# Kernel tuning notes

Measured on AMD Instinct MI355X. Metric: run time of the kernel, lower is better.

## Reference

```python
import jax, jax.numpy as jnp
import numpy as np

D, C, N = 128, 128, 1000000
NUM_PLACES = 5000
TOPK = 10
MIN_SIM = 0.8
MIN_VOTES = 0.0


def setup_inputs() -> dict:
    key = jax.random.key(0)
    k1, k2, k3, k4, k5, k6 = jax.random.split(key, 6)
    final_boxes = jax.random.uniform(k1, (D, 4), dtype=jnp.float32)
    final_scores = jax.random.uniform(k2, (D,), dtype=jnp.float32)
    final_classes = jax.random.randint(k3, (D,), 0, 80, dtype=jnp.int64)
    descriptors = jax.random.normal(k4, (D, C), dtype=jnp.float32)
    X = jax.random.normal(k5, (N, C), dtype=jnp.float32)
    place_ids = jax.random.randint(k6, (N, 1), 0, NUM_PLACES).astype(jnp.float32)
    places_db = jnp.concatenate([X, place_ids], axis=1)  # (N, C+1)
    return {
        "final_boxes": final_boxes,
        "final_scores": final_scores,
        "final_classes": final_classes,
        "descriptors": descriptors,
        "places_db": places_db,
    }


def reference(final_boxes, final_scores, final_classes, descriptors, places_db):
    X = places_db[:, :-1]                       # (N, C)
    idx = places_db[:, -1].astype(jnp.int32)    # (N,) place ids

    sims = jnp.matmul(descriptors, X.T)         # (D, N)  -- dominant traffic
    top_sims, top_idx = jax.lax.top_k(sims, TOPK)  # (D, K)

    places = idx[top_idx]                       # (D, K) place ids of neighbors
    mask = top_sims >= MIN_SIM                  # (D, K) accepted neighbors

    # per-row vote counts: for each kept entry i, count kept entries with same id
    eq = places[:, :, None] == places[:, None, :]          # (D, K, K)
    counts = jnp.sum(eq & mask[:, None, :], axis=2)        # (D, K)
    counts = jnp.where(mask, counts, 0)

    max_count = counts.max(axis=1)                          # (D,)
    n_kept = mask.sum(axis=1)                               # (D,)

    # torch.unique sorts ids ascending, counts.argmax picks first max ->
    # tie-break by smallest place id among entries with max count
    BIG = jnp.int32(2**30)
    cand = mask & (counts == max_count[:, None])
    majority = jnp.where(cand, places, BIG).min(axis=1)     # (D,)

    vote_ratio = max_count.astype(jnp.float32) / jnp.maximum(n_kept, 1).astype(jnp.float32)
    valid = (n_kept > 0) & (vote_ratio >= MIN_VOTES)

    classes_out = jnp.where(valid, majority, -1).astype(jnp.int64)

    # similarity score: max top_sim whose neighbor id equals the majority
    # (over ALL topk entries, regardless of min_sim mask, as in original)
    match = places == jnp.where(valid, majority, -1)[:, None]
    NEG = jnp.float32(-1e30)
    best = jnp.where(match, top_sims, NEG).max(axis=1)
    scores_out = jnp.where(valid & match.any(axis=1), best, 0.0).astype(jnp.float32)

    return final_boxes, scores_out, classes_out
```

## Files before the change

kernel.cpp:

```cpp
#include <hip/hip_runtime.h>
#include <stdint.h>

#define DQ 128
#define CDIM 128
#define ROW_F 129
#define N_DB 1000000
#define CHUNK 32
#define NCHUNK (N_DB / CHUNK)
#define GRIDF 768
#define NTHRF 256
#define CHUNK_FLOATS (CHUNK * ROW_F)
#define WAVE_SLOTS 258
#define BF_STRIDE 136
#define BFB_SHORTS (CHUNK * BF_STRIDE)
#define CAP 512
#define NTOP 10
#define MIN_SIM_F 0.8f

typedef __attribute__((ext_vector_type(8))) short bf16x8;
typedef __attribute__((ext_vector_type(4))) float f32x4;
typedef __attribute__((ext_vector_type(4))) uint32_t u32x4;

#define AS1 __attribute__((address_space(1)))
#define AS3 __attribute__((address_space(3)))

__device__ __forceinline__ short f2bf_rne(float x) {
  uint32_t u = __float_as_uint(x);
  u += 0x7FFFu + ((u >> 16) & 1u);
  return (short)(u >> 16);
}

__device__ __forceinline__ void stage32(const float* __restrict__ src,
                                        float* scr, int w, int lane) {
  const int base = w * WAVE_SLOTS;
#pragma unroll
  for (int k = 0; k < 4; ++k) {
    const int s = base + 64 * k + lane;
    __builtin_amdgcn_global_load_lds((const AS1 void*)(src + 4 * s),
                                     (AS3 void*)(scr + 4 * (base + 64 * k)),
                                     16, 0, 0);
  }
  if (lane < 2) {
    const int s = base + 256 + lane;
    __builtin_amdgcn_global_load_lds((const AS1 void*)(src + 4 * s),
                                     (AS3 void*)(scr + 4 * (base + 256)),
                                     16, 0, 0);
  }
}

__device__ __forceinline__ void pack32(const float* scr, short* bfb, int w,
                                       int lane) {
  const int r = 8 * w + (lane >> 3);
  const int cb = lane & 7;
  const float* rp = scr + r * ROW_F + cb * 16;
  uint32_t d[8];
#pragma unroll
  for (int i = 0; i < 8; ++i) {
    const uint32_t ue = __float_as_uint(rp[2 * i]);
    const uint32_t uo = __float_as_uint(rp[2 * i + 1]);
    d[i] = __builtin_amdgcn_perm(uo, ue, 0x07060302u);
  }
  u32x4* wp = (u32x4*)(bfb + r * BF_STRIDE + cb * 16);
  wp[0] = (u32x4){d[0], d[1], d[2], d[3]};
  wp[1] = (u32x4){d[4], d[5], d[6], d[7]};
}

__global__ __launch_bounds__(NTHRF, 4) void filter_kernel(
    const float* __restrict__ desc, const float* __restrict__ pdb,
    int* __restrict__ cnt, int* __restrict__ cand) {
  __shared__ float tau_s[DQ];
  __shared__ __align__(16) float scr0[CHUNK_FLOATS];
  __shared__ __align__(16) float scr1[CHUNK_FLOATS];
  __shared__ __align__(16) short bfb0[BFB_SHORTS];
  __shared__ __align__(16) short bfb1[BFB_SHORTS];

  const int t = threadIdx.x;
  const int w = t >> 6;
  const int lane = t & 63;
  const int r16 = lane & 15;
  const int kg = lane >> 4;

  const int bid = blockIdx.x;
  const int C = (NCHUNK - bid + GRIDF - 1) / GRIDF;

  if (t < DQ) {
    const float4* dp = (const float4*)(desc + t * CDIM);
    float ssq = 0.f;
#pragma unroll
    for (int c = 0; c < 32; ++c) {
      const float4 v = dp[c];
      ssq = fmaf(v.x, v.x, ssq);
      ssq = fmaf(v.y, v.y, ssq);
      ssq = fmaf(v.z, v.z, ssq);
      ssq = fmaf(v.w, v.w, ssq);
    }
    tau_s[t] = 3.8f * sqrtf(ssq) - 2.0f;
  }

  bf16x8 afrag[2][4];
#pragma unroll
  for (int qt = 0; qt < 2; ++qt) {
    const int q = (2 * w + qt) * 16 + r16;
#pragma unroll
    for (int ks = 0; ks < 4; ++ks) {
      const float* ap = desc + q * CDIM + ks * 32 + kg * 8;
      bf16x8 a;
#pragma unroll
      for (int j = 0; j < 8; ++j) a[j] = f2bf_rne(ap[j]);
      afrag[qt][ks] = a;
    }
  }

  asm volatile("s_waitcnt vmcnt(0)" ::: "memory");

  stage32(pdb + (size_t)bid * CHUNK_FLOATS, scr0, w, lane);
  if (C > 1) {
    stage32(pdb + (size_t)(bid + GRIDF) * CHUNK_FLOATS, scr1, w, lane);
    asm volatile("s_waitcnt vmcnt(5)" ::: "memory");
  } else {
    asm volatile("s_waitcnt vmcnt(0)" ::: "memory");
  }
  pack32(scr0, bfb0, w, lane);
  asm volatile("s_waitcnt lgkmcnt(0)" ::: "memory");
  __builtin_amdgcn_s_barrier();
  asm volatile("" ::: "memory");

  float tau_l[2][4];
#pragma unroll
  for (int qt = 0; qt < 2; ++qt)
#pragma unroll
    for (int r = 0; r < 4; ++r)
      tau_l[qt][r] = tau_s[(2 * w + qt) * 16 + kg * 4 + r];

  for (int i = 0; i < C; ++i) {
    const int chunk = bid + i * GRIDF;
    float* scr_st = (i & 1) ? scr1 : scr0;
    const float* scr_pk = (i & 1) ? scr0 : scr1;
    const short* bf_cm = (i & 1) ? bfb1 : bfb0;
    short* bf_pk = (i & 1) ? bfb0 : bfb1;
    const bool have2 = (i + 2 < C);

    if (have2)
      stage32(pdb + (size_t)(chunk + 2 * GRIDF) * CHUNK_FLOATS, scr_st, w, lane);

    f32x4 acc[2][2];
    acc[0][0] = (f32x4){0.f, 0.f, 0.f, 0.f};
    acc[0][1] = (f32x4){0.f, 0.f, 0.f, 0.f};
    acc[1][0] = (f32x4){0.f, 0.f, 0.f, 0.f};
    acc[1][1] = (f32x4){0.f, 0.f, 0.f, 0.f};
#pragma unroll
    for (int ks = 0; ks < 4; ++ks) {
#pragma unroll
      for (int rt = 0; rt < 2; ++rt) {
        const bf16x8 b =
            *(const bf16x8*)(bf_cm + (rt * 16 + r16) * BF_STRIDE + ks * 32 + kg * 8);
        acc[0][rt] =
            __builtin_amdgcn_mfma_f32_16x16x32_bf16(afrag[0][ks], b, acc[0][rt], 0, 0, 0);
        acc[1][rt] =
            __builtin_amdgcn_mfma_f32_16x16x32_bf16(afrag[1][ks], b, acc[1][rt], 0, 0, 0);
      }
    }

#pragma unroll
    for (int qt = 0; qt < 2; ++qt)
#pragma unroll
      for (int rt = 0; rt < 2; ++rt)
#pragma unroll
        for (int reg = 0; reg < 4; ++reg) {
          const float sim = acc[qt][rt][reg];
          if (sim >= tau_l[qt][reg]) {
            const int q = (2 * w + qt) * 16 + kg * 4 + reg;
            const int row = chunk * CHUNK + rt * 16 + r16;
            const int pos = atomicAdd(&cnt[q], 1);
            if (pos < CAP) cand[q * CAP + pos] = row;
          }
        }

    if (have2)
      asm volatile("s_waitcnt vmcnt(5)" ::: "memory");
    else
      asm volatile("s_waitcnt vmcnt(0)" ::: "memory");

    if (i + 1 < C) pack32(scr_pk, bf_pk, w, lane);

    asm volatile("s_waitcnt lgkmcnt(0)" ::: "memory");
    __builtin_amdgcn_s_barrier();
    asm volatile("" ::: "memory");
  }
}

__global__ __launch_bounds__(512) void finalize_kernel(
    const float* __restrict__ boxes, const float* __restrict__ desc,
    const float* __restrict__ pdb, const int* __restrict__ cnt,
    const int* __restrict__ cand, float* __restrict__ out) {
  const int q = blockIdx.x;
  const int t = threadIdx.x;
  const int wav = t >> 6;
  const int lane = t & 63;
  __shared__ float dq[CDIM];
  __shared__ float simsL[CAP];
  __shared__ int idxL[CAP];

  if (t < CDIM) dq[t] = desc[q * CDIM + t];
  __syncthreads();

  int n = cnt[q];
  if (n > CAP) n = CAP;

  const float dql = dq[lane];
  const float dqh = dq[lane + 64];
  const int base_q = q * CAP;

  for (int ci0 = wav; ci0 < n; ci0 += 32) {
    int r[4];
#pragma unroll
    for (int u = 0; u < 4; ++u) {
      const int ci = ci0 + 8 * u;
      r[u] = cand[base_q + ((ci < n) ? ci : ci0)];
    }
    float a[4], b[4];
#pragma unroll
    for (int u = 0; u < 4; ++u) {
      const float* xp = pdb + (size_t)r[u] * ROW_F;
      a[u] = xp[lane];
      b[u] = xp[lane + 64];
    }
#pragma unroll
    for (int u = 0; u < 4; ++u) {
      const int ci = ci0 + 8 * u;
      float part = fmaf(dql, a[u], dqh * b[u]);
#pragma unroll
      for (int off = 32; off; off >>= 1) part += __shfl_xor(part, off);
      if (ci < n && lane == 0) {
        simsL[ci] = part;
        idxL[ci] = r[u];
      }
    }
  }
  __syncthreads();

  if (t < 4) out[q * 4 + t] = boxes[q * 4 + t];

  if (wav == 0) {
    float ts[NTOP];
    int ti[NTOP];
#pragma unroll
    for (int k = 0; k < NTOP; ++k) {
      float bv = -3e38f;
      int ba = -1;
      for (int ci = lane; ci < n; ci += 64)
        if (simsL[ci] > bv) { bv = simsL[ci]; ba = ci; }
#pragma unroll
      for (int off = 32; off; off >>= 1) {
        const float ov = __shfl_xor(bv, off);
        const int oa = __shfl_xor(ba, off);
        if (ov > bv) { bv = ov; ba = oa; }
      }
      ts[k] = bv;
      ti[k] = (ba >= 0) ? idxL[ba] : -1;
      if (lane == 0 && ba >= 0) simsL[ba] = -3e38f;
    }

    if (lane == 0) {
      int pl[NTOP];
      bool mk[NTOP];
      int n_kept = 0;
#pragma unroll
      for (int k = 0; k < NTOP; ++k) {
        pl[k] = (ti[k] >= 0) ? (int)pdb[(size_t)ti[k] * ROW_F + CDIM] : -2;
        mk[k] = (ti[k] >= 0) && (ts[k] >= MIN_SIM_F);
        n_kept += mk[k] ? 1 : 0;
      }
      int maxc = 0;
      int counts[NTOP];
#pragma unroll
      for (int j = 0; j < NTOP; ++j) {
        int cj = 0;
        if (mk[j]) {
#pragma unroll
          for (int k = 0; k < NTOP; ++k)
            if (mk[k] && pl[k] == pl[j]) cj++;
        }
        counts[j] = cj;
        if (cj > maxc) maxc = cj;
      }
      const int BIGC = 1 << 30;
      int majority = BIGC;
#pragma unroll
      for (int j = 0; j < NTOP; ++j)
        if (mk[j] && counts[j] == maxc && pl[j] < majority) majority = pl[j];
      const bool valid = (n_kept > 0);
      const int cls = valid ? majority : -1;
      bool any = false;
      float best = -3e38f;
#pragma unroll
      for (int k = 0; k < NTOP; ++k)
        if (pl[k] == cls) {
          any = true;
          if (ts[k] > best) best = ts[k];
        }
      const float score = (valid && any) ? best : 0.f;
      out[512 + q] = score;
      out[640 + q] = (float)cls;
    }
  }
}

extern "C" void kernel_launch(void* const* d_in, const int* in_sizes, int n_in,
                              void* d_out, int out_size, void* d_ws,
                              size_t ws_size, hipStream_t stream) {
  (void)in_sizes; (void)n_in; (void)out_size; (void)ws_size;
  const float* boxes = (const float*)d_in[0];
  const float* desc = (const float*)d_in[3];
  const float* pdb = (const float*)d_in[4];
  float* out = (float*)d_out;

  int* cnt = (int*)d_ws;
  int* cand = (int*)((char*)d_ws + 512);

  hipMemsetAsync(cnt, 0, DQ * sizeof(int), stream);
  filter_kernel<<<GRIDF, NTHRF, 0, stream>>>(desc, pdb, cnt, cand);
  finalize_kernel<<<DQ, 512, 0, stream>>>(boxes, desc, pdb, cnt, cand, out);
}
```

Baseline: 141.0 us.

## Stage database chunks through registers instead of direct global-to-LDS loads

Replaces the async global_load_lds staging with ordinary float4 loads into two sets of registers, prefetched two chunks ahead, which are then written to LDS scratch and packed to bf16. The main loop is unrolled by two to ping-pong register sets and LDS buffers explicitly. The first database loads are issued before the descriptor norm and fragment setup so they overlap that work. This adds register pressure, so launch bounds drop from 4 to 3 blocks per CU, and the extra LDS write and wait per chunk could reduce latency hiding.

```diff
diff --git a/kernel.cpp b/kernel.cpp
--- a/kernel.cpp
+++ b/kernel.cpp
@@ -10,7 +10,6 @@
 #define GRIDF 768
 #define NTHRF 256
 #define CHUNK_FLOATS (CHUNK * ROW_F)
-#define WAVE_SLOTS 258
 #define BF_STRIDE 136
 #define BFB_SHORTS (CHUNK * BF_STRIDE)
 #define CAP 512
@@ -21,31 +20,10 @@
 typedef __attribute__((ext_vector_type(4))) float f32x4;
 typedef __attribute__((ext_vector_type(4))) uint32_t u32x4;
 
-#define AS1 __attribute__((address_space(1)))
-#define AS3 __attribute__((address_space(3)))
-
 __device__ __forceinline__ short f2bf_rne(float x) {
   uint32_t u = __float_as_uint(x);
   u += 0x7FFFu + ((u >> 16) & 1u);
   return (short)(u >> 16);
-}
-
-__device__ __forceinline__ void stage32(const float* __restrict__ src,
-                                        float* scr, int w, int lane) {
-  const int base = w * WAVE_SLOTS;
-#pragma unroll
-  for (int k = 0; k < 4; ++k) {
-    const int s = base + 64 * k + lane;
-    __builtin_amdgcn_global_load_lds((const AS1 void*)(src + 4 * s),
-                                     (AS3 void*)(scr + 4 * (base + 64 * k)),
-                                     16, 0, 0);
-  }
-  if (lane < 2) {
-    const int s = base + 256 + lane;
-    __builtin_amdgcn_global_load_lds((const AS1 void*)(src + 4 * s),
-                                     (AS3 void*)(scr + 4 * (base + 256)),
-                                     16, 0, 0);
-  }
 }
 
 __device__ __forceinline__ void pack32(const float* scr, short* bfb, int w,
@@ -65,7 +43,65 @@
   wp[1] = (u32x4){d[4], d[5], d[6], d[7]};
 }
 
-__global__ __launch_bounds__(NTHRF, 4) void filter_kernel(
+#define LOADS(cc, R0, R1, R2, R3, RT)                                          \
+  do {                                                                         \
+    const float4* ps_ =                                                        \
+        (const float4*)(pdb + (size_t)(cc)*CHUNK_FLOATS) + 258 * w;            \
+    R0 = ps_[lane];                                                            \
+    R1 = ps_[64 + lane];                                                       \
+    R2 = ps_[128 + lane];                                                      \
+    R3 = ps_[192 + lane];                                                      \
+    if (lane < 2) RT = ps_[256 + lane];                                        \
+  } while (0)
+
+#define WRITES(scr_, R0, R1, R2, R3, RT)                                       \
+  do {                                                                         \
+    float4* qs_ = (float4*)(scr_) + 258 * w;                                   \
+    qs_[lane] = R0;                                                            \
+    qs_[64 + lane] = R1;                                                       \
+    qs_[128 + lane] = R2;                                                      \
+    qs_[192 + lane] = R3;                                                      \
+    if (lane < 2) qs_[256 + lane] = RT;                                        \
+  } while (0)
+
+#define LGKM0() asm volatile("s_waitcnt lgkmcnt(0)" ::: "memory")
+#define BARRIER()                                                              \
+  do {                                                                         \
+    __builtin_amdgcn_s_barrier();                                              \
+    asm volatile("" ::: "memory");                                             \
+  } while (0)
+
+#define COMPUTE_CHUNK(bf_cm, chunkidx)                                         \
+  do {                                                                         \
+    f32x4 acc[2][2];                                                           \
+    acc[0][0] = (f32x4){0.f, 0.f, 0.f, 0.f};                                   \
+    acc[0][1] = (f32x4){0.f, 0.f, 0.f, 0.f};                                   \
+    acc[1][0] = (f32x4){0.f, 0.f, 0.f, 0.f};                                   \
+    acc[1][1] = (f32x4){0.f, 0.f, 0.f, 0.f};                                   \
+    _Pragma("unroll") for (int ks = 0; ks < 4; ++ks) {                         \
+      _Pragma("unroll") for (int rt = 0; rt < 2; ++rt) {                       \
+        const bf16x8 b = *(const bf16x8*)((bf_cm) + (rt * 16 + r16) *          \
+                                              BF_STRIDE + ks * 32 + kg * 8);   \
+        acc[0][rt] = __builtin_amdgcn_mfma_f32_16x16x32_bf16(                  \
+            afrag[0][ks], b, acc[0][rt], 0, 0, 0);                             \
+        acc[1][rt] = __builtin_amdgcn_mfma_f32_16x16x32_bf16(                  \
+            afrag[1][ks], b, acc[1][rt], 0, 0, 0);                             \
+      }                                                                        \
+    }                                                                          \
+    _Pragma("unroll") for (int qt = 0; qt < 2; ++qt)                           \
+        _Pragma("unroll") for (int rt = 0; rt < 2; ++rt)                       \
+            _Pragma("unroll") for (int reg = 0; reg < 4; ++reg) {              \
+      const float sim = acc[qt][rt][reg];                                      \
+      if (sim >= tau_l[qt][reg]) {                                             \
+        const int q = (2 * w + qt) * 16 + kg * 4 + reg;                        \
+        const int row = (chunkidx)*CHUNK + rt * 16 + r16;                      \
+        const int pos = atomicAdd(&cnt[q], 1);                                 \
+        if (pos < CAP) cand[q * CAP + pos] = row;                              \
+      }                                                                        \
+    }                                                                          \
+  } while (0)
+
+__global__ __launch_bounds__(NTHRF, 3) void filter_kernel(
     const float* __restrict__ desc, const float* __restrict__ pdb,
     int* __restrict__ cnt, int* __restrict__ cand) {
   __shared__ float tau_s[DQ];
@@ -83,6 +119,12 @@
   const int bid = blockIdx.x;
   const int C = (NCHUNK - bid + GRIDF - 1) / GRIDF;
 
+  float4 rA0{}, rA1{}, rA2{}, rA3{}, rAt{};
+  float4 rB0{}, rB1{}, rB2{}, rB3{}, rBt{};
+
+  LOADS(bid, rA0, rA1, rA2, rA3, rAt);
+  if (C > 1) LOADS(bid + GRIDF, rB0, rB1, rB2, rB3, rBt);
+
   if (t < DQ) {
     const float4* dp = (const float4*)(desc + t * CDIM);
     float ssq = 0.f;
@@ -111,19 +153,11 @@
     }
   }
 
-  asm volatile("s_waitcnt vmcnt(0)" ::: "memory");
-
-  stage32(pdb + (size_t)bid * CHUNK_FLOATS, scr0, w, lane);
-  if (C > 1) {
-    stage32(pdb + (size_t)(bid + GRIDF) * CHUNK_FLOATS, scr1, w, lane);
-    asm volatile("s_waitcnt vmcnt(5)" ::: "memory");
-  } else {
-    asm volatile("s_waitcnt vmcnt(0)" ::: "memory");
-  }
+  WRITES(scr0, rA0, rA1, rA2, rA3, rAt);
+  LGKM0();
   pack32(scr0, bfb0, w, lane);
-  asm volatile("s_waitcnt lgkmcnt(0)" ::: "memory");
-  __builtin_amdgcn_s_barrier();
-  asm volatile("" ::: "memory");
+  LGKM0();
+  BARRIER();
 
   float tau_l[2][4];
 #pragma unroll
@@ -132,60 +166,27 @@
     for (int r = 0; r < 4; ++r)
       tau_l[qt][r] = tau_s[(2 * w + qt) * 16 + kg * 4 + r];
 
-  for (int i = 0; i < C; ++i) {
-    const int chunk = bid + i * GRIDF;
-    float* scr_st = (i & 1) ? scr1 : scr0;
-    const float* scr_pk = (i & 1) ? scr0 : scr1;
-    const short* bf_cm = (i & 1) ? bfb1 : bfb0;
-    short* bf_pk = (i & 1) ? bfb0 : bfb1;
-    const bool have2 = (i + 2 < C);
-
-    if (have2)
-      stage32(pdb + (size_t)(chunk + 2 * GRIDF) * CHUNK_FLOATS, scr_st, w, lane);
-
-    f32x4 acc[2][2];
-    acc[0][0] = (f32x4){0.f, 0.f, 0.f, 0.f};
-    acc[0][1] = (f32x4){0.f, 0.f, 0.f, 0.f};
-    acc[1][0] = (f32x4){0.f, 0.f, 0.f, 0.f};
-    acc[1][1] = (f32x4){0.f, 0.f, 0.f, 0.f};
-#pragma unroll
-    for (int ks = 0; ks < 4; ++ks) {
-#pragma unroll
-      for (int rt = 0; rt < 2; ++rt) {
-        const bf16x8 b =
-            *(const bf16x8*)(bf_cm + (rt * 16 + r16) * BF_STRIDE + ks * 32 + kg * 8);
-        acc[0][rt] =
-            __builtin_amdgcn_mfma_f32_16x16x32_bf16(afrag[0][ks], b, acc[0][rt], 0, 0, 0);
-        acc[1][rt] =
-            __builtin_amdgcn_mfma_f32_16x16x32_bf16(afrag[1][ks], b, acc[1][rt], 0, 0, 0);
-      }
-    }
-
-#pragma unroll
-    for (int qt = 0; qt < 2; ++qt)
-#pragma unroll
-      for (int rt = 0; rt < 2; ++rt)
-#pragma unroll
-        for (int reg = 0; reg < 4; ++reg) {
-          const float sim = acc[qt][rt][reg];
-          if (sim >= tau_l[qt][reg]) {
-            const int q = (2 * w + qt) * 16 + kg * 4 + reg;
-            const int row = chunk * CHUNK + rt * 16 + r16;
-            const int pos = atomicAdd(&cnt[q], 1);
-            if (pos < CAP) cand[q * CAP + pos] = row;
-          }
-        }
-
-    if (have2)
-      asm volatile("s_waitcnt vmcnt(5)" ::: "memory");
-    else
-      asm volatile("s_waitcnt vmcnt(0)" ::: "memory");
-
-    if (i + 1 < C) pack32(scr_pk, bf_pk, w, lane);
-
-    asm volatile("s_waitcnt lgkmcnt(0)" ::: "memory");
-    __builtin_amdgcn_s_barrier();
-    asm volatile("" ::: "memory");
+  for (int i = 0; i < C; i += 2) {
+    if (i + 2 < C) LOADS(bid + (size_t)(i + 2) * GRIDF, rA0, rA1, rA2, rA3, rAt);
+    COMPUTE_CHUNK(bfb0, bid + i * GRIDF);
+    if (i + 1 < C) {
+      WRITES(scr1, rB0, rB1, rB2, rB3, rBt);
+      LGKM0();
+      pack32(scr1, bfb1, w, lane);
+    }
+    LGKM0();
+    BARRIER();
+    if (i + 1 >= C) break;
+
+    if (i + 3 < C) LOADS(bid + (size_t)(i + 3) * GRIDF, rB0, rB1, rB2, rB3, rBt);
+    COMPUTE_CHUNK(bfb1, bid + (i + 1) * GRIDF);
+    if (i + 2 < C) {
+      WRITES(scr0, rA0, rA1, rA2, rA3, rAt);
+      LGKM0();
+      pack32(scr0, bfb0, w, lane);
+    }
+    LGKM0();
+    BARRIER();
   }
 }
 
```

After: 132.4 us. 6.1% less time.
